# Kernel optimization log

Measured on AMD Instinct MI355X. Metric: run time of the kernel, lower is better.

The kernel has to match this reference:

```python
import jax, jax.numpy as jnp
import numpy as np

BOUNDS = (0, 256, 384, 448, 512)  # rot_idx, trans_idx, angle_idx, embedding_dim
SCALES = [1, 2, 4, 8, 16, 32, 64]  # 2**i for i in range(scales+1), scales=6


def _pairwise_dist(q, e):
    # q: [M, C] queries, e: [K, C] codebook; per-segment squared dist / seg_dim, summed
    d = jnp.zeros((q.shape[0], e.shape[0]), dtype=q.dtype)
    for s, t in zip(BOUNDS[:-1], BOUNDS[1:]):
        qs, es = q[:, s:t], e[:, s:t]
        d = d + (jnp.sum(qs * qs, axis=1, keepdims=True)
                 + jnp.sum(es * es, axis=1)
                 - 2.0 * qs @ es.T) / (t - s)
    return d


def _elem_dist(q, k):
    # q, k: [B, C, N]; elementwise per-segment squared distance / seg_dim -> [B, N]
    d = 0.0
    for s, t in zip(BOUNDS[:-1], BOUNDS[1:]):
        diff = q[:, s:t] - k[:, s:t]
        d = d + jnp.sum(diff * diff, axis=1) / (t - s)
    return d


def _downsample_area(f, pn):
    # f: [B, C, N], pn divides N -> block-mean pooling (torch 'area')
    B, C, N = f.shape
    return f.reshape(B, C, pn, N // pn).mean(axis=-1)


def _upsample_linear(h, N):
    # h: [B, C, pn] -> [B, C, N], torch mode='linear', align_corners=False
    pn = h.shape[-1]
    src = (jnp.arange(N, dtype=jnp.float32) + 0.5) * (pn / N) - 0.5
    src = jnp.clip(src, 0.0, pn - 1)
    i0 = jnp.floor(src).astype(jnp.int32)
    i1 = jnp.minimum(i0 + 1, pn - 1)
    w = (src - i0).astype(h.dtype)
    return h[..., i0] * (1.0 - w) + h[..., i1] * w


def setup_inputs() -> dict:
    key = jax.random.key(0)
    k1, k2, k3 = jax.random.split(key, 3)
    C = 512
    f_BNC = jax.random.normal(k1, (1024, 64, C), dtype=jnp.float32)
    base = jax.random.normal(k2, (2048, C), dtype=jnp.float32)
    proj_W = jax.random.normal(k3, (C, C), dtype=jnp.float32) / np.sqrt(C)
    return {"f_BNC": f_BNC, "base": base, "proj_W": proj_W}


def reference(f_BNC, base, proj_W):
    embedding = base @ proj_W.T              # update_embedding(): proj(base)
    emb_ng = jax.lax.stop_gradient(embedding)
    f_BCN = jnp.transpose(f_BNC, (0, 2, 1))  # [B, C, N]
    B, C, N = f_BCN.shape
    f_no_grad = jax.lax.stop_gradient(f_BCN)
    f_rest = f_no_grad
    f_hat = jnp.zeros_like(f_rest)
    commit = jnp.zeros((B, N), dtype=f_BCN.dtype)
    qlat = jnp.zeros((B, N), dtype=f_BCN.dtype)
    for pn in SCALES:
        rest_NC = jnp.transpose(_downsample_area(f_rest, pn), (0, 2, 1)).reshape(-1, C)
        d = _pairwise_dist(jax.lax.stop_gradient(rest_NC), emb_ng)  # [B*pn, K]
        idx = jnp.argmin(d, axis=1)
        h_NC = embedding[idx]                                        # gather (grad -> codebook)
        h_BCn = jnp.transpose(h_NC.reshape(B, pn, C), (0, 2, 1))
        h_BCN = _upsample_linear(h_BCn, N)
        f_hat = f_hat + h_BCN
        f_rest = f_rest - h_BCN
        commit = commit + 0.25 * _elem_dist(jax.lax.stop_gradient(f_hat), f_BCN)
        qlat = qlat + _elem_dist(f_hat, f_no_grad)
    SN = float(len(SCALES))
    commit = commit / SN
    qlat = qlat / SN
    f_hat_st = jax.lax.stop_gradient(f_hat) - f_no_grad + f_BCN  # straight-through
    return (jnp.transpose(f_hat_st, (0, 2, 1)), commit, qlat)
```

## Files before the change

kernel.cpp:

```cpp
#include <hip/hip_runtime.h>

typedef __attribute__((ext_vector_type(8))) _Float16 f16x8;
typedef __attribute__((ext_vector_type(4))) float f32x4;

#define B_    1024
#define C_    512
#define NCODE 2048
#define NTOT  (B_ * 64 * C_)
#define BN_   (B_ * 64)
#define DELTA 6e-3f

__device__ __forceinline__ float wseg(int k) {
    return k < 256 ? (1.0f / 256.0f) : (k < 384 ? (1.0f / 128.0f) : (1.0f / 64.0f));
}

__device__ __forceinline__ unsigned packkey(float s, int code) {
    unsigned u = __float_as_uint(s);
    u = (u & 0x80000000u) ? ~u : (u | 0x80000000u);
    return (u & 0xFFFFF800u) | (unsigned)code;
}
__device__ __forceinline__ float unpk(unsigned k) {
    unsigned us = k & 0xFFFFF800u;
    return (us & 0x80000000u) ? __uint_as_float(us ^ 0x80000000u) : __uint_as_float(~us);
}

__global__ __launch_bounds__(256) void k_gemm_e(const float* __restrict__ A,
                                                const float* __restrict__ Bm,
                                                float* __restrict__ E,
                                                _Float16* __restrict__ wk) {
    __shared__ float As[16][68];
    __shared__ float Bs[16][68];
    int tid = threadIdx.x;
    int m0 = blockIdx.x * 64, n0 = blockIdx.y * 64;
    float acc[4][4] = {};
    int tx = tid & 15, ty = tid >> 4;
    int kk = tid & 15, rr = tid >> 4;
    for (int k0 = 0; k0 < 512; k0 += 16) {
        #pragma unroll
        for (int i = 0; i < 4; ++i) {
            As[kk][rr + i * 16] = A[(m0 + rr + i * 16) * 512 + k0 + kk];
            Bs[kk][rr + i * 16] = Bm[(n0 + rr + i * 16) * 512 + k0 + kk];
        }
        __syncthreads();
        #pragma unroll
        for (int k = 0; k < 16; ++k) {
            float4 a = *(const float4*)&As[k][ty * 4];
            float4 b = *(const float4*)&Bs[k][tx * 4];
            #pragma unroll
            for (int i = 0; i < 4; ++i) {
                float av = ((const float*)&a)[i];
                acc[i][0] = fmaf(av, b.x, acc[i][0]);
                acc[i][1] = fmaf(av, b.y, acc[i][1]);
                acc[i][2] = fmaf(av, b.z, acc[i][2]);
                acc[i][3] = fmaf(av, b.w, acc[i][3]);
            }
        }
        __syncthreads();
    }
    #pragma unroll
    for (int i = 0; i < 4; ++i)
        #pragma unroll
        for (int j = 0; j < 4; ++j) {
            int cc = m0 + ty * 4 + i;
            int kx = n0 + tx * 4 + j;
            float v = acc[i][j];
            E[cc * 512 + kx] = v;
            wk[cc * 512 + kx] = (_Float16)(v * wseg(kx));
        }
}

__global__ void k_enorm(const float* __restrict__ E, float* __restrict__ enorm) {
    int c = blockIdx.x * 256 + threadIdx.x;
    float s = 0.0f;
    for (int k = 0; k < 512; ++k) {
        float v = E[c * 512 + k];
        s = fmaf(wseg(k) * v, v, s);
    }
    enorm[c] = s;
}

__global__ __launch_bounds__(256) void k_down0(const float* __restrict__ f,
                                               _Float16* __restrict__ q16,
                                               float* __restrict__ qf) {
    int b = blockIdx.x, t = threadIdx.x;
    const float* src = f + (size_t)b * 64 * 512;
    float s0 = 0.f, s1 = 0.f;
    for (int n = 0; n < 64; ++n) {
        s0 += src[n * 512 + t];
        s1 += src[n * 512 + t + 256];
    }
    s0 *= (1.0f / 64.0f); s1 *= (1.0f / 64.0f);
    q16[(size_t)b * 512 + t] = (_Float16)s0;
    q16[(size_t)b * 512 + t + 256] = (_Float16)s1;
    qf[(size_t)b * 512 + t] = s0;
    qf[(size_t)b * 512 + t + 256] = s1;
}

#define GLL2(gp, loff) __builtin_amdgcn_global_load_lds( \
    (const __attribute__((address_space(1))) unsigned int*)(gp), \
    (__attribute__((address_space(3))) unsigned int*)(smem + (loff)), 16, 0, 0)

__global__ __launch_bounds__(512, 2) void k_score_256(
        const _Float16* __restrict__ q16, const _Float16* __restrict__ wek,
        const float* __restrict__ enorm, float4* __restrict__ partial) {
    extern __shared__ char smem[];
    int tid = threadIdx.x;
    int x = blockIdx.x;
    int bx = (x >> 3) & 7;
    int g  = (x & 7) + ((x >> 6) << 3);
    int m0 = g * 256, n0 = bx * 256;

    int lane = tid & 63, wave = tid >> 6;
    int wm = wave >> 2, wn = wave & 3;
    int lx = lane & 15, cg = lane >> 4;

    int r2s = tid >> 3, sl = tid & 7;
    int us = sl ^ (r2s & 7);
    int cs = us & 3;
    int rws = r2s + ((us >> 2) << 6);
    const _Float16* srcA0 = q16 + (size_t)(m0 + rws) * 512 + cs * 8;
    const _Float16* srcA1 = q16 + (size_t)(m0 + 128 + rws) * 512 + cs * 8;
    const _Float16* srcB0 = wek + (size_t)(n0 + rws) * 512 + cs * 8;
    const _Float16* srcB1 = wek + (size_t)(n0 + 128 + rws) * 512 + cs * 8;

    #define STG_A(BUF, RH, KT) { const _Float16* s_ = ((RH) ? srcA1 : srcA0) + (KT) * 64; \
        GLL2(s_,      (BUF) * 65536 +     0 + (RH) * 8192 + tid * 16); \
        GLL2(s_ + 32, (BUF) * 65536 + 16384 + (RH) * 8192 + tid * 16); }
    #define STG_B(BUF, RH, KT) { const _Float16* s_ = ((RH) ? srcB1 : srcB0) + (KT) * 64; \
        GLL2(s_,      (BUF) * 65536 + 32768 + (RH) * 8192 + tid * 16); \
        GLL2(s_ + 32, (BUF) * 65536 + 49152 + (RH) * 8192 + tid * 16); }

    int Aoff[8];
    #pragma unroll
    for (int fi = 0; fi < 8; ++fi) {
        int rA = fi * 16 + lx;
        Aoff[fi] = wm * 8192 + (rA & 63) * 128 +
                   (((((rA >> 6) & 1) << 2) + cg) ^ (rA & 7)) * 16;
    }
    int Boff[4];
    #pragma unroll
    for (int fj = 0; fj < 4; ++fj) {
        int br = wn * 64 + fj * 16 + lx;
        int rB = br & 127;
        Boff[fj] = 32768 + (br >> 7) * 8192 + (rB & 63) * 128 +
                   (((((rB >> 6) & 1) << 2) + cg) ^ (rB & 7)) * 16;
    }

    f32x4 acc[8][4];
    #pragma unroll
    for (int i = 0; i < 8; ++i)
        #pragma unroll
        for (int j = 0; j < 4; ++j)
            acc[i][j] = (f32x4){0.f, 0.f, 0.f, 0.f};

    f16x8 bf00, bf01, bf10, bf11, bf20, bf21, bf30, bf31;
    #define LDB(BUF) \
        bf00 = *(const f16x8*)(smem + (BUF) * 65536 +         Boff[0]); \
        bf01 = *(const f16x8*)(smem + (BUF) * 65536 + 16384 + Boff[0]); \
        bf10 = *(const f16x8*)(smem + (BUF) * 65536 +         Boff[1]); \
        bf11 = *(const f16x8*)(smem + (BUF) * 65536 + 16384 + Boff[1]); \
        bf20 = *(const f16x8*)(smem + (BUF) * 65536 +         Boff[2]); \
        bf21 = *(const f16x8*)(smem + (BUF) * 65536 + 16384 + Boff[2]); \
        bf30 = *(const f16x8*)(smem + (BUF) * 65536 +         Boff[3]); \
        bf31 = *(const f16x8*)(smem + (BUF) * 65536 + 16384 + Boff[3]);

    #define MF(a, b, c) __builtin_amdgcn_mfma_f32_16x16x32_f16(a, b, c, 0, 0, 0)
    #define PH(BUF, F0, STAGE, VMW) { \
        f16x8 aA0 = *(const f16x8*)(smem + (BUF) * 65536 +         Aoff[F0]); \
        f16x8 aA1 = *(const f16x8*)(smem + (BUF) * 65536 + 16384 + Aoff[F0]); \
        f16x8 aB0 = *(const f16x8*)(smem + (BUF) * 65536 +         Aoff[(F0) + 1]); \
        f16x8 aB1 = *(const f16x8*)(smem + (BUF) * 65536 + 16384 + Aoff[(F0) + 1]); \
        STAGE; VMW; \
        __builtin_amdgcn_s_barrier(); \
        __builtin_amdgcn_s_setprio(1); \
        acc[F0][0] = MF(aA0, bf00, acc[F0][0]); acc[F0][0] = MF(aA1, bf01, acc[F0][0]); \
        acc[F0][1] = MF(aA0, bf10, acc[F0][1]); acc[F0][1] = MF(aA1, bf11, acc[F0][1]); \
        acc[F0][2] = MF(aA0, bf20, acc[F0][2]); acc[F0][2] = MF(aA1, bf21, acc[F0][2]); \
        acc[F0][3] = MF(aA0, bf30, acc[F0][3]); acc[F0][3] = MF(aA1, bf31, acc[F0][3]); \
        acc[(F0)+1][0] = MF(aB0, bf00, acc[(F0)+1][0]); acc[(F0)+1][0] = MF(aB1, bf01, acc[(F0)+1][0]); \
        acc[(F0)+1][1] = MF(aB0, bf10, acc[(F0)+1][1]); acc[(F0)+1][1] = MF(aB1, bf11, acc[(F0)+1][1]); \
        acc[(F0)+1][2] = MF(aB0, bf20, acc[(F0)+1][2]); acc[(F0)+1][2] = MF(aB1, bf21, acc[(F0)+1][2]); \
        acc[(F0)+1][3] = MF(aB0, bf30, acc[(F0)+1][3]); acc[(F0)+1][3] = MF(aB1, bf31, acc[(F0)+1][3]); \
        __builtin_amdgcn_s_setprio(0); \
        __builtin_amdgcn_s_barrier(); \
    }

    STG_A(0, 0, 0); STG_A(0, 1, 0); STG_B(0, 0, 0); STG_B(0, 1, 0);
    STG_B(1, 0, 1); STG_B(1, 1, 1); STG_A(1, 0, 1);
    asm volatile("s_waitcnt vmcnt(6)" ::: "memory");
    __builtin_amdgcn_s_barrier();

    #pragma unroll
    for (int it = 0; it < 4; ++it) {
        const int t0 = 2 * it, t1 = 2 * it + 1;
        LDB(0);
        PH(0, 0, STG_A(1, 1, t1), );
        PH(0, 2, if (it < 3) STG_B(0, 0, t0 + 2), );
        PH(0, 4, if (it < 3) STG_B(0, 1, t0 + 2), );
        PH(0, 6, if (it < 3) STG_A(0, 0, t0 + 2),
                 if (it < 3) { asm volatile("s_waitcnt vmcnt(6)" ::: "memory"); }
                 else        { asm volatile("s_waitcnt vmcnt(0)" ::: "memory"); });
        LDB(1);
        PH(1, 0, if (it < 3) STG_A(0, 1, t0 + 2), );
        PH(1, 2, if (it < 3) STG_B(1, 0, t0 + 3), );
        PH(1, 4, if (it < 3) STG_B(1, 1, t0 + 3), );
        PH(1, 6, if (it < 3) STG_A(1, 0, t0 + 3),
                 if (it < 3) { asm volatile("s_waitcnt vmcnt(6)" ::: "memory"); }
                 else        { asm volatile("s_waitcnt vmcnt(0)" ::: "memory"); });
    }

    float en[4];
    #pragma unroll
    for (int fj = 0; fj < 4; ++fj) en[fj] = enorm[n0 + wn * 64 + fj * 16 + lx];

    #pragma unroll
    for (int fi = 0; fi < 8; ++fi) {
        #pragma unroll
        for (int rr = 0; rr < 4; ++rr) {
            unsigned a1 = 0xFFFFFFFFu, a2 = 0xFFFFFFFFu;
            #pragma unroll
            for (int fj = 0; fj < 4; ++fj) {
                float s = fmaf(-2.0f, acc[fi][fj][rr], en[fj]);
                unsigned key = packkey(s, n0 + wn * 64 + fj * 16 + lx);
                if (key < a1) { a2 = a1; a1 = key; }
                else if (key < a2) a2 = key;
            }
            #pragma unroll
            for (int d = 1; d < 16; d <<= 1) {
                unsigned b1 = (unsigned)__shfl_xor((int)a1, d);
                unsigned b2 = (unsigned)__shfl_xor((int)a2, d);
                if (b1 < a1) { a2 = min(a1, b2); a1 = b1; }
                else a2 = min(a2, b1);
            }
            if (lx == 0) {
                int row = m0 + wm * 128 + fi * 16 + cg * 4 + rr;
                partial[(size_t)row * 32 + (bx * 4 + wn)] =
                    make_float4(unpk(a1), __int_as_float((int)(a1 & 2047u)),
                                unpk(a2), __int_as_float((int)(a2 & 2047u)));
            }
        }
    }
    #undef STG_A
    #undef STG_B
    #undef LDB
    #undef PH
    #undef MF
}

__global__ __launch_bounds__(256) void k_score_f16(
        const _Float16* __restrict__ q16, const _Float16* __restrict__ wek,
        const float* __restrict__ enorm, float4* __restrict__ partial) {
    __shared__ __align__(16) char smem[37376];
    float*  ensh = (float*)(smem + 32768);
    float4* bb   = (float4*)(smem + 33280);

    int tid = threadIdx.x;
    int x = blockIdx.x;
    int bx = (x >> 3) & 15;
    int g  = (x & 7) + ((x >> 7) << 3);
    int m0 = g * 128, n0 = bx * 128;
    if (tid < 128) ensh[tid] = enorm[n0 + tid];

    int lane = tid & 63, wave = tid >> 6;
    int wrow = (wave & 1) * 64, wcol = (wave >> 1) * 64;
    int lx = lane & 15, cg = lane >> 4;

    int u = (tid & 7) ^ ((tid >> 3) & 7);
    int chunk = u & 3;
    int rhi = (u >> 2) << 6;
    int r0 = (tid >> 3) + rhi;
    int r1 = 32 + (tid >> 3) + rhi;
    const _Float16* gqa0 = q16 + (size_t)(m0 + r0) * 512 + chunk * 8;
    const _Float16* gqa1 = q16 + (size_t)(m0 + r1) * 512 + chunk * 8;
    const _Float16* gwb0 = wek + (size_t)(n0 + r0) * 512 + chunk * 8;
    const _Float16* gwb1 = wek + (size_t)(n0 + r1) * 512 + chunk * 8;

    auto stage = [&](int buf, int k0) {
        GLL2(gqa0 + k0, buf * 16384 + tid * 16);
        GLL2(gqa1 + k0, buf * 16384 + 4096 + tid * 16);
        GLL2(gwb0 + k0, buf * 16384 + 8192 + tid * 16);
        GLL2(gwb1 + k0, buf * 16384 + 12288 + tid * 16);
    };

    f32x4 acc[4][4];
    #pragma unroll
    for (int i = 0; i < 4; ++i)
        #pragma unroll
        for (int j = 0; j < 4; ++j)
            acc[i][j] = (f32x4){0.f, 0.f, 0.f, 0.f};

    int swzA = (((wrow >> 6) * 4 + cg) ^ (lx & 7)) * 16;
    int swzB = (((wcol >> 6) * 4 + cg) ^ (lx & 7)) * 16;
    int abase = lx * 128 + swzA;
    int bbase = 8192 + lx * 128 + swzB;

    stage(0, 0);
    __syncthreads();

    #pragma unroll
    for (int ks = 0; ks < 16; ++ks) {
        int p = ks & 1;
        if (ks < 15) stage(p ^ 1, (ks + 1) * 32);
        f16x8 af[4], bf[4];
        #pragma unroll
        for (int i = 0; i < 4; ++i) {
            af[i] = *(const f16x8*)(smem + p * 16384 + abase + i * 2048);
            bf[i] = *(const f16x8*)(smem + p * 16384 + bbase + i * 2048);
        }
        #pragma unroll
        for (int i = 0; i < 4; ++i)
            #pragma unroll
            for (int j = 0; j < 4; ++j)
                acc[i][j] = __builtin_amdgcn_mfma_f32_16x16x32_f16(af[i], bf[j], acc[i][j], 0, 0, 0);
        __syncthreads();
    }

    #pragma unroll
    for (int fi = 0; fi < 4; ++fi) {
        #pragma unroll
        for (int r = 0; r < 4; ++r) {
            float v1 = INFINITY, v2 = INFINITY; int i1 = NCODE, i2 = NCODE;
            #pragma unroll
            for (int fj = 0; fj < 4; ++fj) {
                int nl = wcol + fj * 16 + lx;
                float s = ensh[nl] - 2.0f * acc[fi][fj][r];
                int code = n0 + nl;
                if (s < v1) { v2 = v1; i2 = i1; v1 = s; i1 = code; }
                else if (s < v2) { v2 = s; i2 = code; }
            }
            #pragma unroll
            for (int d = 1; d < 16; d <<= 1) {
                float ov1 = __shfl_xor(v1, d), ov2 = __shfl_xor(v2, d);
                int oi1 = __shfl_xor(i1, d), oi2 = __shfl_xor(i2, d);
                if (ov1 < v1) {
                    if (v1 < ov2) { v2 = v1; i2 = i1; } else { v2 = ov2; i2 = oi2; }
                    v1 = ov1; i1 = oi1;
                } else if (ov1 < v2) { v2 = ov1; i2 = oi1; }
            }
            if (lx == 0) {
                int row = wrow + fi * 16 + cg * 4 + r;
                bb[row * 2 + (wave >> 1)] = make_float4(v1, __int_as_float(i1),
                                                        v2, __int_as_float(i2));
            }
        }
    }
    __syncthreads();
    if (tid < 128) {
        float4 A4 = bb[tid * 2], C4 = bb[tid * 2 + 1];
        float v1, v2; int i1, i2;
        if (A4.x <= C4.x) {
            v1 = A4.x; i1 = __float_as_int(A4.y);
            if (A4.z <= C4.x) { v2 = A4.z; i2 = __float_as_int(A4.w); }
            else { v2 = C4.x; i2 = __float_as_int(C4.y); }
        } else {
            v1 = C4.x; i1 = __float_as_int(C4.y);
            if (C4.z <= A4.x) { v2 = C4.z; i2 = __float_as_int(C4.w); }
            else { v2 = A4.x; i2 = __float_as_int(A4.y); }
        }
        partial[(size_t)(m0 + tid) * 16 + bx] =
            make_float4(v1, __int_as_float(i1), v2, __int_as_float(i2));
    }
}

__global__ __launch_bounds__(256) void k_rescue(
        const float4* __restrict__ partial, const float* __restrict__ qf,
        const float* __restrict__ E, const float* __restrict__ enorm,
        int* __restrict__ idxb, int nslots) {
    int wid = (blockIdx.x * 256 + threadIdx.x) >> 6;
    int lane = threadIdx.x & 63;
    float4 p;
    if (lane < nslots) p = partial[(size_t)wid * nslots + lane];
    else p = make_float4(INFINITY, __int_as_float(NCODE), INFINITY, __int_as_float(NCODE));
    float bv = p.x;
    #pragma unroll
    for (int d = 1; d < 64; d <<= 1) bv = fminf(bv, __shfl_xor(bv, d));
    float thresh = bv + DELTA;
    unsigned long long m1 = __ballot(lane < nslots && p.x <= thresh);
    unsigned long long m2 = __ballot(lane < nslots && p.z <= thresh);
    const float* q = qf + (size_t)wid * 512 + lane * 8;
    float4 q0 = *(const float4*)q;
    float4 q1 = *(const float4*)(q + 4);
    float w = wseg(lane * 8);
    float qw0 = q0.x * w, qw1 = q0.y * w, qw2 = q0.z * w, qw3 = q0.w * w;
    float qw4 = q1.x * w, qw5 = q1.y * w, qw6 = q1.z * w, qw7 = q1.w * w;
    float bs = INFINITY; int bi = NCODE;
    while (m1 | m2) {
        int ci;
        if (m1) {
            int src = __ffsll((long long)m1) - 1; m1 &= m1 - 1;
            ci = __shfl(__float_as_int(p.y), src);
        } else {
            int src = __ffsll((long long)m2) - 1; m2 &= m2 - 1;
            ci = __shfl(__float_as_int(p.w), src);
        }
        const float* e = E + (size_t)ci * 512 + lane * 8;
        float4 e0 = *(const float4*)e;
        float4 e1 = *(const float4*)(e + 4);
        float a = 0.f;
        a = fmaf(qw0, e0.x, a); a = fmaf(qw1, e0.y, a);
        a = fmaf(qw2, e0.z, a); a = fmaf(qw3, e0.w, a);
        a = fmaf(qw4, e1.x, a); a = fmaf(qw5, e1.y, a);
        a = fmaf(qw6, e1.z, a); a = fmaf(qw7, e1.w, a);
        #pragma unroll
        for (int d = 1; d < 64; d <<= 1) a += __shfl_xor(a, d);
        float s = enorm[ci] - 2.0f * a;
        if (s < bs || (s == bs && ci < bi)) { bs = s; bi = ci; }
    }
    if (lane == 0) idxb[wid] = bi;
}

__global__ __launch_bounds__(256) void k_update(
        const float* __restrict__ E, const int* __restrict__ idx,
        const float* __restrict__ f, float* __restrict__ rest,
        float* __restrict__ dacc, _Float16* __restrict__ q16n,
        float* __restrict__ qf32n, int pn, int sn, int mode) {
    int t = threadIdx.x;
    int pn_next = 1 << sn;
    int r = 64 >> sn;
    int b = blockIdx.x >> sn;
    int chunk = blockIdx.x & (pn_next - 1);
    int lane = t & 63, wave = t >> 6;
    int col = wave * 128 + lane * 2;
    float w0 = wseg(col);
    float macc0 = 0.f, macc1 = 0.f;
    float pscale = (float)pn * (1.0f / 64.0f);
    __shared__ float daccP[32][5];
    #pragma unroll 1
    for (int ri = 0; ri < r; ++ri) {
        int n = chunk * r + ri;
        int row = (b << 6) + n;
        float srcp = fminf(fmaxf((n + 0.5f) * pscale - 0.5f, 0.0f), (float)(pn - 1));
        int i0 = (int)floorf(srcp);
        int i1 = min(i0 + 1, pn - 1);
        float wl = srcp - (float)i0;
        int cc0 = idx[b * pn + i0];
        int cc1 = idx[b * pn + i1];
        float2 e0 = *(const float2*)(E + (size_t)cc0 * 512 + col);
        float2 e1 = *(const float2*)(E + (size_t)cc1 * 512 + col);
        size_t off = (size_t)row * 512 + col;
        float2 rv = (mode & 1) ? *(const float2*)(f + off)
                               : *(const float2*)(rest + off);
        float h0 = (1.0f - wl) * e0.x + wl * e1.x;
        float h1 = (1.0f - wl) * e0.y + wl * e1.y;
        float v0 = rv.x - h0, v1 = rv.y - h1;
        float2 wout;
        if (mode & 2) {
            float2 fv = *(const float2*)(f + off);
            wout = make_float2(fv.x - v0, fv.y - v1);
        } else {
            wout = make_float2(v0, v1);
        }
        *(float2*)(rest + off) = wout;
        float s = fmaf(w0 * v0, v0, w0 * v1 * v1);
        #pragma unroll
        for (int d = 1; d < 64; d <<= 1) s += __shfl_xor(s, d);
        if (lane == 0) daccP[ri][wave] = s;
        macc0 += v0; macc1 += v1;
    }
    __syncthreads();
    if (t < r) {
        int row = (b << 6) + chunk * r + t;
        float tot = daccP[t][0] + daccP[t][1] + daccP[t][2] + daccP[t][3];
        dacc[row] = (mode & 1) ? tot : dacc[row] + tot;
    }
    if (!(mode & 2)) {
        float inv = 1.0f / (float)r;
        size_t qrow = ((size_t)b << sn) + chunk;
        float m0v = macc0 * inv, m1v = macc1 * inv;
        q16n[qrow * 512 + col] = (_Float16)m0v;
        q16n[qrow * 512 + col + 1] = (_Float16)m1v;
        if (mode & 4) {
            *(float2*)(qf32n + qrow * 512 + col) = make_float2(m0v, m1v);
        }
    }
}

__global__ void k_out12(const float* __restrict__ dacc, float* __restrict__ out) {
    int i = blockIdx.x * 256 + threadIdx.x;
    float d = dacc[i];
    out[i] = d * (0.25f / 7.0f);
    out[BN_ + i] = d * (1.0f / 7.0f);
}

extern "C" void kernel_launch(void* const* d_in, const int* in_sizes, int n_in,
                              void* d_out, int out_size, void* d_ws, size_t ws_size,
                              hipStream_t stream) {
    const float* f    = (const float*)d_in[0];
    const float* base = (const float*)d_in[1];
    const float* W    = (const float*)d_in[2];
    float* out = (float*)d_out;
    float* rest = out;

    char* ws = (char*)d_ws;
    float*     E      = (float*)ws;     ws += (size_t)NCODE * 512 * 4;
    _Float16*  wek16  = (_Float16*)ws;  ws += (size_t)NCODE * 512 * 2;
    _Float16*  q16a   = (_Float16*)ws;  ws += (size_t)32768 * 512 * 2;
    char*      big64  = ws;             ws += (size_t)65536 * 512 * 2;
    float4*    partS  = (float4*)ws;    ws += (size_t)32768 * 32 * 16;
    float*     dacc   = (float*)ws;     ws += (size_t)BN_ * 4;
    int*       idxb   = (int*)ws;       ws += (size_t)BN_ * 4;
    float*     enorm  = (float*)ws;     ws += (size_t)NCODE * 4;

    k_gemm_e<<<dim3(NCODE / 64, 512 / 64), 256, 0, stream>>>(base, W, E, wek16);
    k_enorm<<<NCODE / 256, 256, 0, stream>>>(E, enorm);
    k_down0<<<B_, 256, 0, stream>>>(f, q16a, (float*)big64);

    const int scales[7] = {1, 2, 4, 8, 16, 32, 64};
    for (int si = 0; si < 7; ++si) {
        int pn = scales[si];
        int M = 1024 * pn;
        const _Float16* q16s = (pn == 64) ? (const _Float16*)big64 : q16a;
        const float*    qfs  = (pn == 64) ? rest : (const float*)big64;

        if (pn >= 8) {
            float4* part = (pn == 64) ? (float4*)q16a : partS;
            k_score_256<<<8 * (M / 256), 512, 131072, stream>>>(q16s, wek16, enorm, part);
            k_rescue<<<M / 4, 256, 0, stream>>>(part, qfs, E, enorm, idxb, 32);
        } else {
            k_score_f16<<<16 * (M / 128), 256, 0, stream>>>(q16s, wek16, enorm, partS);
            k_rescue<<<M / 4, 256, 0, stream>>>(partS, qfs, E, enorm, idxb, 16);
        }

        int pn_next = (si == 6) ? 64 : pn * 2;
        int sn = 0; while ((1 << sn) != pn_next) ++sn;
        int mode = (si == 0 ? 1 : 0) | (si == 6 ? 2 : 0) | ((si <= 4) ? 4 : 0);
        _Float16* q16n = (pn_next == 64) ? (_Float16*)big64 : q16a;
        k_update<<<1024 * pn_next, 256, 0, stream>>>(E, idxb, f, rest, dacc,
                                                     q16n, (float*)big64, pn, sn, mode);
    }

    k_out12<<<BN_ / 256, 256, 0, stream>>>(dacc, out + NTOT);
}
```

Before: 1.025 ms.

## Deepen score GEMM pipeline to 4 K-stages and pack partial top-2 keys

The main score GEMM moves from a 2-buffer, 64-wide K step to a 4-buffer, 32-wide K step with three tiles in flight, issuing A and B stage loads between two MFMA half-phases. The epilogue drops the 16-lane shuffle top-2 reduction and instead writes per-lane candidates to LDS, then reduces them with a per-thread scan. Partial results shrink from float4 to packed uint2 keys, halving partial traffic in the score and rescue kernels. Packing truncates the low score bits, which could slightly change which candidates fall inside the rescue threshold, and the extra barriers per K step may add sync overhead.

```diff
diff --git a/kernel.cpp b/kernel.cpp
--- a/kernel.cpp
+++ b/kernel.cpp
@@ -102,7 +102,7 @@
 
 __global__ __launch_bounds__(512, 2) void k_score_256(
         const _Float16* __restrict__ q16, const _Float16* __restrict__ wek,
-        const float* __restrict__ enorm, float4* __restrict__ partial) {
+        const float* __restrict__ enorm, uint2* __restrict__ partial) {
     extern __shared__ char smem[];
     int tid = threadIdx.x;
     int x = blockIdx.x;
@@ -123,12 +123,12 @@
     const _Float16* srcB0 = wek + (size_t)(n0 + rws) * 512 + cs * 8;
     const _Float16* srcB1 = wek + (size_t)(n0 + 128 + rws) * 512 + cs * 8;
 
-    #define STG_A(BUF, RH, KT) { const _Float16* s_ = ((RH) ? srcA1 : srcA0) + (KT) * 64; \
-        GLL2(s_,      (BUF) * 65536 +     0 + (RH) * 8192 + tid * 16); \
-        GLL2(s_ + 32, (BUF) * 65536 + 16384 + (RH) * 8192 + tid * 16); }
-    #define STG_B(BUF, RH, KT) { const _Float16* s_ = ((RH) ? srcB1 : srcB0) + (KT) * 64; \
-        GLL2(s_,      (BUF) * 65536 + 32768 + (RH) * 8192 + tid * 16); \
-        GLL2(s_ + 32, (BUF) * 65536 + 49152 + (RH) * 8192 + tid * 16); }
+    #define STG_A2(BUF, KT) { \
+        GLL2(srcA0 + (KT) * 32, (BUF) * 32768 + tid * 16); \
+        GLL2(srcA1 + (KT) * 32, (BUF) * 32768 + 8192 + tid * 16); }
+    #define STG_B2(BUF, KT) { \
+        GLL2(srcB0 + (KT) * 32, (BUF) * 32768 + 16384 + tid * 16); \
+        GLL2(srcB1 + (KT) * 32, (BUF) * 32768 + 24576 + tid * 16); }
 
     int Aoff[8];
     #pragma unroll
@@ -142,7 +142,7 @@
     for (int fj = 0; fj < 4; ++fj) {
         int br = wn * 64 + fj * 16 + lx;
         int rB = br & 127;
-        Boff[fj] = 32768 + (br >> 7) * 8192 + (rB & 63) * 128 +
+        Boff[fj] = 16384 + (br >> 7) * 8192 + (rB & 63) * 128 +
                    (((((rB >> 6) & 1) << 2) + cg) ^ (rB & 7)) * 16;
     }
 
@@ -153,62 +153,62 @@
         for (int j = 0; j < 4; ++j)
             acc[i][j] = (f32x4){0.f, 0.f, 0.f, 0.f};
 
-    f16x8 bf00, bf01, bf10, bf11, bf20, bf21, bf30, bf31;
-    #define LDB(BUF) \
-        bf00 = *(const f16x8*)(smem + (BUF) * 65536 +         Boff[0]); \
-        bf01 = *(const f16x8*)(smem + (BUF) * 65536 + 16384 + Boff[0]); \
-        bf10 = *(const f16x8*)(smem + (BUF) * 65536 +         Boff[1]); \
-        bf11 = *(const f16x8*)(smem + (BUF) * 65536 + 16384 + Boff[1]); \
-        bf20 = *(const f16x8*)(smem + (BUF) * 65536 +         Boff[2]); \
-        bf21 = *(const f16x8*)(smem + (BUF) * 65536 + 16384 + Boff[2]); \
-        bf30 = *(const f16x8*)(smem + (BUF) * 65536 +         Boff[3]); \
-        bf31 = *(const f16x8*)(smem + (BUF) * 65536 + 16384 + Boff[3]);
-
     #define MF(a, b, c) __builtin_amdgcn_mfma_f32_16x16x32_f16(a, b, c, 0, 0, 0)
-    #define PH(BUF, F0, STAGE, VMW) { \
-        f16x8 aA0 = *(const f16x8*)(smem + (BUF) * 65536 +         Aoff[F0]); \
-        f16x8 aA1 = *(const f16x8*)(smem + (BUF) * 65536 + 16384 + Aoff[F0]); \
-        f16x8 aB0 = *(const f16x8*)(smem + (BUF) * 65536 +         Aoff[(F0) + 1]); \
-        f16x8 aB1 = *(const f16x8*)(smem + (BUF) * 65536 + 16384 + Aoff[(F0) + 1]); \
-        STAGE; VMW; \
-        __builtin_amdgcn_s_barrier(); \
-        __builtin_amdgcn_s_setprio(1); \
-        acc[F0][0] = MF(aA0, bf00, acc[F0][0]); acc[F0][0] = MF(aA1, bf01, acc[F0][0]); \
-        acc[F0][1] = MF(aA0, bf10, acc[F0][1]); acc[F0][1] = MF(aA1, bf11, acc[F0][1]); \
-        acc[F0][2] = MF(aA0, bf20, acc[F0][2]); acc[F0][2] = MF(aA1, bf21, acc[F0][2]); \
-        acc[F0][3] = MF(aA0, bf30, acc[F0][3]); acc[F0][3] = MF(aA1, bf31, acc[F0][3]); \
-        acc[(F0)+1][0] = MF(aB0, bf00, acc[(F0)+1][0]); acc[(F0)+1][0] = MF(aB1, bf01, acc[(F0)+1][0]); \
-        acc[(F0)+1][1] = MF(aB0, bf10, acc[(F0)+1][1]); acc[(F0)+1][1] = MF(aB1, bf11, acc[(F0)+1][1]); \
-        acc[(F0)+1][2] = MF(aB0, bf20, acc[(F0)+1][2]); acc[(F0)+1][2] = MF(aB1, bf21, acc[(F0)+1][2]); \
-        acc[(F0)+1][3] = MF(aB0, bf30, acc[(F0)+1][3]); acc[(F0)+1][3] = MF(aB1, bf31, acc[(F0)+1][3]); \
-        __builtin_amdgcn_s_setprio(0); \
-        __builtin_amdgcn_s_barrier(); \
-    }
-
-    STG_A(0, 0, 0); STG_A(0, 1, 0); STG_B(0, 0, 0); STG_B(0, 1, 0);
-    STG_B(1, 0, 1); STG_B(1, 1, 1); STG_A(1, 0, 1);
-    asm volatile("s_waitcnt vmcnt(6)" ::: "memory");
+
+    STG_A2(0, 0); STG_B2(0, 0);
+    STG_A2(1, 1); STG_B2(1, 1);
+    STG_A2(2, 2); STG_B2(2, 2);
+    asm volatile("s_waitcnt vmcnt(8)" ::: "memory");
     __builtin_amdgcn_s_barrier();
 
     #pragma unroll
-    for (int it = 0; it < 4; ++it) {
-        const int t0 = 2 * it, t1 = 2 * it + 1;
-        LDB(0);
-        PH(0, 0, STG_A(1, 1, t1), );
-        PH(0, 2, if (it < 3) STG_B(0, 0, t0 + 2), );
-        PH(0, 4, if (it < 3) STG_B(0, 1, t0 + 2), );
-        PH(0, 6, if (it < 3) STG_A(0, 0, t0 + 2),
-                 if (it < 3) { asm volatile("s_waitcnt vmcnt(6)" ::: "memory"); }
-                 else        { asm volatile("s_waitcnt vmcnt(0)" ::: "memory"); });
-        LDB(1);
-        PH(1, 0, if (it < 3) STG_A(0, 1, t0 + 2), );
-        PH(1, 2, if (it < 3) STG_B(1, 0, t0 + 3), );
-        PH(1, 4, if (it < 3) STG_B(1, 1, t0 + 3), );
-        PH(1, 6, if (it < 3) STG_A(1, 0, t0 + 3),
-                 if (it < 3) { asm volatile("s_waitcnt vmcnt(6)" ::: "memory"); }
-                 else        { asm volatile("s_waitcnt vmcnt(0)" ::: "memory"); });
-    }
-
+    for (int t = 0; t < 16; ++t) {
+        const int buf = (t & 3) * 32768;
+        const int sb = (t + 3) & 3;
+        f16x8 a0 = *(const f16x8*)(smem + buf + Aoff[0]);
+        f16x8 a1 = *(const f16x8*)(smem + buf + Aoff[1]);
+        f16x8 a2 = *(const f16x8*)(smem + buf + Aoff[2]);
+        f16x8 a3 = *(const f16x8*)(smem + buf + Aoff[3]);
+        f16x8 b0 = *(const f16x8*)(smem + buf + Boff[0]);
+        f16x8 b1 = *(const f16x8*)(smem + buf + Boff[1]);
+        f16x8 b2 = *(const f16x8*)(smem + buf + Boff[2]);
+        f16x8 b3 = *(const f16x8*)(smem + buf + Boff[3]);
+        if (t < 13) STG_A2(sb, t + 3);
+        __builtin_amdgcn_s_barrier();
+        __builtin_amdgcn_s_setprio(1);
+        acc[0][0] = MF(a0, b0, acc[0][0]); acc[0][1] = MF(a0, b1, acc[0][1]);
+        acc[0][2] = MF(a0, b2, acc[0][2]); acc[0][3] = MF(a0, b3, acc[0][3]);
+        acc[1][0] = MF(a1, b0, acc[1][0]); acc[1][1] = MF(a1, b1, acc[1][1]);
+        acc[1][2] = MF(a1, b2, acc[1][2]); acc[1][3] = MF(a1, b3, acc[1][3]);
+        acc[2][0] = MF(a2, b0, acc[2][0]); acc[2][1] = MF(a2, b1, acc[2][1]);
+        acc[2][2] = MF(a2, b2, acc[2][2]); acc[2][3] = MF(a2, b3, acc[2][3]);
+        acc[3][0] = MF(a3, b0, acc[3][0]); acc[3][1] = MF(a3, b1, acc[3][1]);
+        acc[3][2] = MF(a3, b2, acc[3][2]); acc[3][3] = MF(a3, b3, acc[3][3]);
+        __builtin_amdgcn_s_setprio(0);
+        __builtin_amdgcn_s_barrier();
+        f16x8 a4 = *(const f16x8*)(smem + buf + Aoff[4]);
+        f16x8 a5 = *(const f16x8*)(smem + buf + Aoff[5]);
+        f16x8 a6 = *(const f16x8*)(smem + buf + Aoff[6]);
+        f16x8 a7 = *(const f16x8*)(smem + buf + Aoff[7]);
+        if (t < 13) STG_B2(sb, t + 3);
+        if (t < 13)      { asm volatile("s_waitcnt vmcnt(8)" ::: "memory"); }
+        else if (t == 13){ asm volatile("s_waitcnt vmcnt(4)" ::: "memory"); }
+        else if (t == 14){ asm volatile("s_waitcnt vmcnt(0)" ::: "memory"); }
+        __builtin_amdgcn_s_barrier();
+        __builtin_amdgcn_s_setprio(1);
+        acc[4][0] = MF(a4, b0, acc[4][0]); acc[4][1] = MF(a4, b1, acc[4][1]);
+        acc[4][2] = MF(a4, b2, acc[4][2]); acc[4][3] = MF(a4, b3, acc[4][3]);
+        acc[5][0] = MF(a5, b0, acc[5][0]); acc[5][1] = MF(a5, b1, acc[5][1]);
+        acc[5][2] = MF(a5, b2, acc[5][2]); acc[5][3] = MF(a5, b3, acc[5][3]);
+        acc[6][0] = MF(a6, b0, acc[6][0]); acc[6][1] = MF(a6, b1, acc[6][1]);
+        acc[6][2] = MF(a6, b2, acc[6][2]); acc[6][3] = MF(a6, b3, acc[6][3]);
+        acc[7][0] = MF(a7, b0, acc[7][0]); acc[7][1] = MF(a7, b1, acc[7][1]);
+        acc[7][2] = MF(a7, b2, acc[7][2]); acc[7][3] = MF(a7, b3, acc[7][3]);
+        __builtin_amdgcn_s_setprio(0);
+        __builtin_amdgcn_s_barrier();
+    }
+
+    __syncthreads();
     float en[4];
     #pragma unroll
     for (int fj = 0; fj < 4; ++fj) en[fj] = enorm[n0 + wn * 64 + fj * 16 + lx];
@@ -225,31 +225,33 @@
                 if (key < a1) { a2 = a1; a1 = key; }
                 else if (key < a2) a2 = key;
             }
-            #pragma unroll
-            for (int d = 1; d < 16; d <<= 1) {
-                unsigned b1 = (unsigned)__shfl_xor((int)a1, d);
-                unsigned b2 = (unsigned)__shfl_xor((int)a2, d);
-                if (b1 < a1) { a2 = min(a1, b2); a1 = b1; }
-                else a2 = min(a2, b1);
-            }
-            if (lx == 0) {
-                int row = m0 + wm * 128 + fi * 16 + cg * 4 + rr;
-                partial[(size_t)row * 32 + (bx * 4 + wn)] =
-                    make_float4(unpk(a1), __int_as_float((int)(a1 & 2047u)),
-                                unpk(a2), __int_as_float((int)(a2 & 2047u)));
-            }
-        }
-    }
-    #undef STG_A
-    #undef STG_B
-    #undef LDB
-    #undef PH
+            int row_local = wm * 128 + fi * 16 + cg * 4 + rr;
+            int task = row_local * 4 + wn;
+            *(uint2*)(smem + task * 128 + ((lx ^ (task & 15)) * 8)) = make_uint2(a1, a2);
+        }
+    }
+    __syncthreads();
+    #pragma unroll
+    for (int rep = 0; rep < 2; ++rep) {
+        int task = tid + rep * 512;
+        unsigned a1 = 0xFFFFFFFFu, a2 = 0xFFFFFFFFu;
+        #pragma unroll
+        for (int j = 0; j < 16; ++j) {
+            uint2 pr = *(const uint2*)(smem + task * 128 + (((j ^ (task & 15))) * 8));
+            if (pr.x < a1) { a2 = min(a1, pr.y); a1 = pr.x; }
+            else a2 = min(a2, pr.x);
+        }
+        int row = m0 + (task >> 2);
+        partial[(size_t)row * 32 + (bx * 4 + (task & 3))] = make_uint2(a1, a2);
+    }
+    #undef STG_A2
+    #undef STG_B2
     #undef MF
 }
 
 __global__ __launch_bounds__(256) void k_score_f16(
         const _Float16* __restrict__ q16, const _Float16* __restrict__ wek,
-        const float* __restrict__ enorm, float4* __restrict__ partial) {
+        const float* __restrict__ enorm, uint2* __restrict__ partial) {
     __shared__ __align__(16) char smem[37376];
     float*  ensh = (float*)(smem + 32768);
     float4* bb   = (float4*)(smem + 33280);
@@ -358,25 +360,28 @@
             else { v2 = A4.x; i2 = __float_as_int(A4.y); }
         }
         partial[(size_t)(m0 + tid) * 16 + bx] =
-            make_float4(v1, __int_as_float(i1), v2, __int_as_float(i2));
+            make_uint2(packkey(v1, i1), packkey(v2, i2));
     }
 }
 
 __global__ __launch_bounds__(256) void k_rescue(
-        const float4* __restrict__ partial, const float* __restrict__ qf,
+        const uint2* __restrict__ partial, const float* __restrict__ qf,
         const float* __restrict__ E, const float* __restrict__ enorm,
         int* __restrict__ idxb, int nslots) {
     int wid = (blockIdx.x * 256 + threadIdx.x) >> 6;
     int lane = threadIdx.x & 63;
-    float4 p;
-    if (lane < nslots) p = partial[(size_t)wid * nslots + lane];
-    else p = make_float4(INFINITY, __int_as_float(NCODE), INFINITY, __int_as_float(NCODE));
-    float bv = p.x;
+    unsigned k1 = 0xFFFFFFFFu, k2 = 0xFFFFFFFFu;
+    if (lane < nslots) {
+        uint2 kk = partial[(size_t)wid * nslots + lane];
+        k1 = kk.x; k2 = kk.y;
+    }
+    float v1 = unpk(k1), v2 = unpk(k2);
+    float bv = v1;
     #pragma unroll
     for (int d = 1; d < 64; d <<= 1) bv = fminf(bv, __shfl_xor(bv, d));
     float thresh = bv + DELTA;
-    unsigned long long m1 = __ballot(lane < nslots && p.x <= thresh);
-    unsigned long long m2 = __ballot(lane < nslots && p.z <= thresh);
+    unsigned long long m1 = __ballot(lane < nslots && v1 <= thresh);
+    unsigned long long m2 = __ballot(lane < nslots && v2 <= thresh);
     const float* q = qf + (size_t)wid * 512 + lane * 8;
     float4 q0 = *(const float4*)q;
     float4 q1 = *(const float4*)(q + 4);
@@ -388,10 +393,10 @@
         int ci;
         if (m1) {
             int src = __ffsll((long long)m1) - 1; m1 &= m1 - 1;
-            ci = __shfl(__float_as_int(p.y), src);
+            ci = __shfl((int)k1, src) & 2047;
         } else {
             int src = __ffsll((long long)m2) - 1; m2 &= m2 - 1;
-            ci = __shfl(__float_as_int(p.w), src);
+            ci = __shfl((int)k2, src) & 2047;
         }
         const float* e = E + (size_t)ci * 512 + lane * 8;
         float4 e0 = *(const float4*)e;
@@ -496,7 +501,7 @@
     _Float16*  wek16  = (_Float16*)ws;  ws += (size_t)NCODE * 512 * 2;
     _Float16*  q16a   = (_Float16*)ws;  ws += (size_t)32768 * 512 * 2;
     char*      big64  = ws;             ws += (size_t)65536 * 512 * 2;
-    float4*    partS  = (float4*)ws;    ws += (size_t)32768 * 32 * 16;
+    uint2*     partS  = (uint2*)ws;     ws += (size_t)32768 * 32 * 8;
     float*     dacc   = (float*)ws;     ws += (size_t)BN_ * 4;
     int*       idxb   = (int*)ws;       ws += (size_t)BN_ * 4;
     float*     enorm  = (float*)ws;     ws += (size_t)NCODE * 4;
@@ -513,7 +518,7 @@
         const float*    qfs  = (pn == 64) ? rest : (const float*)big64;
 
         if (pn >= 8) {
-            float4* part = (pn == 64) ? (float4*)q16a : partS;
+            uint2* part = (pn == 64) ? (uint2*)q16a : partS;
             k_score_256<<<8 * (M / 256), 512, 131072, stream>>>(q16s, wek16, enorm, part);
             k_rescue<<<M / 4, 256, 0, stream>>>(part, qfs, E, enorm, idxb, 32);
         } else {
```

New measurement: 984.6 us. 1.04x faster.
